# Optimization experiments

Measured on AMD Instinct MI355X. Metric: run time of the kernel, lower is better.

## Reference

```python
import jax, jax.numpy as jnp
import numpy as np

EPS = 1e-5

def _layernorm(h, g, b):
    m = jnp.mean(h, axis=-1, keepdims=True)
    v = jnp.mean((h - m) ** 2, axis=-1, keepdims=True)
    return (h - m) * jax.lax.rsqrt(v + EPS) * g + b

def setup_inputs() -> dict:
    key = jax.random.key(0)
    ks = jax.random.split(key, 12)
    B, C, T = 8, 512, 8192
    TOK, CD = 256, 768
    s = 0.02
    return {
        "x": jax.random.normal(ks[0], (B, C, T), dtype=jnp.float32),
        "context": jax.random.normal(ks[1], (B, TOK, CD), dtype=jnp.float32),
        "context_mask": jax.random.randint(ks[2], (B, TOK), 0, 2).astype(bool),
        "ln_g": jnp.ones((C,), jnp.float32),
        "ln_b": jnp.zeros((C,), jnp.float32),
        "cln_g": jnp.ones((CD,), jnp.float32),
        "cln_b": jnp.zeros((CD,), jnp.float32),
        "Wq": jax.random.normal(ks[3], (C, C), jnp.float32) * s,
        "bq": jnp.zeros((C,), jnp.float32),
        "Wk": jax.random.normal(ks[4], (C, CD), jnp.float32) * s,
        "bk": jnp.zeros((C,), jnp.float32),
        "Wv": jax.random.normal(ks[5], (C, CD), jnp.float32) * s,
        "bv": jnp.zeros((C,), jnp.float32),
    }

def reference(x, context, context_mask, ln_g, ln_b, cln_g, cln_b, Wq, bq, Wk, bk, Wv, bv):
    H = 8
    B, C, T = x.shape
    TOK = context.shape[1]
    D = C // H
    hidden = jnp.swapaxes(x, 1, 2)                     # [B, T, C]
    q = (_layernorm(hidden, ln_g, ln_b) @ Wq.T + bq).reshape(B, T, H, D)
    ctx_n = _layernorm(context, cln_g, cln_b)          # [B, TOK, CD]
    k = (ctx_n @ Wk.T + bk).reshape(B, TOK, H, D)
    v = (ctx_n @ Wv.T + bv).reshape(B, TOK, H, D)
    q = jax.nn.softmax(q, axis=-1)                     # feature map on queries
    m = context_mask[:, :, None, None]
    k = jnp.where(m, k, -jnp.finfo(k.dtype).max)
    v = v * m.astype(v.dtype)
    k = jax.nn.softmax(k, axis=1)                      # softmax over tokens
    attn = jnp.einsum('bnhd,bnhe->bhde', k, v)         # small [B,H,D,D] context matrix
    out = jnp.einsum('bthd,bhde->bthe', q, attn).reshape(B, T, C)
    return x + jnp.swapaxes(out, 1, 2)
```

## Files before the change

### kernel.cpp

```cpp
#include <hip/hip_runtime.h>

#define B_ 8
#define C_ 512
#define T_ 8192
#define TOK_ 256
#define CD_ 768

typedef __attribute__((ext_vector_type(8))) short bf16x8;
typedef __attribute__((ext_vector_type(4))) float f32x4;

__device__ __forceinline__ unsigned short f2bf(float f){
  union { float f; unsigned u; } v; v.f = f;
  return (unsigned short)((v.u + 0x7FFFu + ((v.u >> 16) & 1u)) >> 16);
}
__device__ __forceinline__ float bf2f(unsigned short h){
  union { unsigned u; float f; } v; v.u = ((unsigned)h) << 16;
  return v.f;
}

__global__ __launch_bounds__(256) void prep(const float* __restrict__ ctx,
    const float* __restrict__ cg_, const float* __restrict__ cb_,
    const float* __restrict__ Wq, const float* __restrict__ Wk, const float* __restrict__ Wv,
    unsigned short* __restrict__ ctx_nb, unsigned short* __restrict__ wq_pk,
    unsigned short* __restrict__ wkv_pk){
  __shared__ float rs[4][2];
  const int bid = blockIdx.x;
  const int tid = threadIdx.x;
  if (bid < 2048){
    const float* p = ctx + (size_t)bid * CD_;
    float s1 = 0.f, s2 = 0.f;
    for (int i = tid; i < CD_; i += 256){ float v = p[i]; s1 += v; s2 += v * v; }
    #pragma unroll
    for (int o = 32; o > 0; o >>= 1){ s1 += __shfl_xor(s1, o); s2 += __shfl_xor(s2, o); }
    if ((tid & 63) == 0){ rs[tid >> 6][0] = s1; rs[tid >> 6][1] = s2; }
    __syncthreads();
    s1 = rs[0][0] + rs[1][0] + rs[2][0] + rs[3][0];
    s2 = rs[0][1] + rs[1][1] + rs[2][1] + rs[3][1];
    float m = s1 / (float)CD_;
    float var = s2 / (float)CD_ - m * m;
    float rstd = rsqrtf(var + 1e-5f);
    unsigned short* q = ctx_nb + (size_t)bid * CD_;
    for (int i = tid; i < CD_; i += 256) q[i] = f2bf((p[i] - m) * rstd * cg_[i] + cb_[i]);
  } else if (bid < 2176){
    int slot = (bid - 2048) * 256 + tid;
    int ln = slot & 63, nt = (slot >> 6) & 31, kk = slot >> 11;
    int n  = nt * 16 + (ln & 15);
    int k0 = kk * 32 + (ln >> 4) * 8;
    bf16x8 v;
    #pragma unroll
    for (int j = 0; j < 8; j++) v[j] = (short)f2bf(Wq[(size_t)n * C_ + k0 + j]);
    *(bf16x8*)&wq_pk[(size_t)slot * 8] = v;
  } else {
    int slot = (bid - 2176) * 256 + tid;
    int ln = slot & 63, nt = (slot >> 6) & 7;
    int kkh = slot >> 9;
    int kk = kkh % 24, h = kkh / 24;
    const float* W = (nt < 4) ? Wk : Wv;
    int row = h * 64 + (nt & 3) * 16 + (ln & 15);
    int k0 = kk * 32 + (ln >> 4) * 8;
    bf16x8 v;
    #pragma unroll
    for (int j = 0; j < 8; j++) v[j] = (short)f2bf(W[(size_t)row * CD_ + k0 + j]);
    *(bf16x8*)&wkv_pk[(size_t)slot * 8] = v;
  }
}

__global__ __launch_bounds__(256) void ctx_attn(const unsigned short* __restrict__ ctx_nb,
    const unsigned short* __restrict__ wkv_pk,
    const float* __restrict__ bk, const float* __restrict__ bv,
    const int* __restrict__ mask, unsigned short* __restrict__ apk){
  __shared__ __align__(16) char smem[75776];
  unsigned short* a_st  = (unsigned short*)smem;
  unsigned short* p_lds = (unsigned short*)smem;
  unsigned short* v_lds = (unsigned short*)(smem + 32768);
  unsigned short* al    = (unsigned short*)(smem + 65536);
  float* wred = (float*)(smem + 73728);
  int* msk_l  = (int*)(smem + 74752);

  const int tid = threadIdx.x;
  const int b = blockIdx.x >> 3, h = blockIdx.x & 7;
  msk_l[tid] = mask[b * 256 + tid];

  const unsigned short* cb = ctx_nb + (size_t)b * 256 * CD_;
  const int w = tid >> 6, ln = tid & 63, lc = ln & 15, lk = ln >> 4;

  {
    const bf16x8* src = (const bf16x8*)(cb + (size_t)tid * CD_);
    #pragma unroll
    for (int s = 0; s < 4; s++){
      bf16x8 vv = src[s];
      *(bf16x8*)&a_st[(tid * 32 + s * 8) ^ ((tid & 7) << 3)] = vv;
    }
  }
  const bf16x8* wv_ = (const bf16x8*)wkv_pk;
  const size_t wbase = (size_t)h * 24 * 8 * 64;
  f32x4 acc[4][8];
  #pragma unroll
  for (int i = 0; i < 4; i++)
    #pragma unroll
    for (int j = 0; j < 8; j++) acc[i][j] = (f32x4){0.f,0.f,0.f,0.f};
  bf16x8 bbuf[2][8];
  #pragma unroll
  for (int nt = 0; nt < 8; nt++) bbuf[0][nt] = wv_[wbase + (size_t)(0 * 8 + nt) * 64 + ln];
  __syncthreads();

  for (int kk = 0; kk < 24; kk++){
    int cur = kk & 1;
    bf16x8 nx[4];
    if (kk < 23){
      const bf16x8* src = (const bf16x8*)(cb + (size_t)tid * CD_ + (kk + 1) * 32);
      #pragma unroll
      for (int s = 0; s < 4; s++) nx[s] = src[s];
      #pragma unroll
      for (int nt = 0; nt < 8; nt++)
        bbuf[cur ^ 1][nt] = wv_[wbase + (size_t)((kk + 1) * 8 + nt) * 64 + ln];
    }
    bf16x8 af[4];
    #pragma unroll
    for (int mt = 0; mt < 4; mt++){
      int row = w * 64 + mt * 16 + lc;
      af[mt] = *(const bf16x8*)&a_st[cur * 8192 + ((row * 32 + lk * 8) ^ ((row & 7) << 3))];
    }
    #pragma unroll
    for (int mt = 0; mt < 4; mt++)
      #pragma unroll
      for (int nt = 0; nt < 8; nt++)
        acc[mt][nt] = __builtin_amdgcn_mfma_f32_16x16x32_bf16(af[mt], bbuf[cur][nt], acc[mt][nt], 0, 0, 0);
    if (kk < 23){
      unsigned short* dst = a_st + (cur ^ 1) * 8192;
      #pragma unroll
      for (int s = 0; s < 4; s++)
        *(bf16x8*)&dst[(tid * 32 + s * 8) ^ ((tid & 7) << 3)] = nx[s];
    }
    __syncthreads();
  }

  float bia[8];
  #pragma unroll
  for (int nt = 0; nt < 8; nt++)
    bia[nt] = (nt < 4) ? bk[h * 64 + nt * 16 + lc] : bv[h * 64 + (nt - 4) * 16 + lc];
  bool mk[4][4];
  #pragma unroll
  for (int mt = 0; mt < 4; mt++)
    #pragma unroll
    for (int r = 0; r < 4; r++)
      mk[mt][r] = msk_l[w * 64 + mt * 16 + lk * 4 + r] != 0;

  float cred[4];
  #pragma unroll
  for (int nt = 0; nt < 4; nt++){
    float mx = -3.402823466e38f;
    #pragma unroll
    for (int mt = 0; mt < 4; mt++)
      #pragma unroll
      for (int r = 0; r < 4; r++)
        if (mk[mt][r]) mx = fmaxf(mx, acc[mt][nt][r] + bia[nt]);
    mx = fmaxf(mx, __shfl_xor(mx, 16));
    mx = fmaxf(mx, __shfl_xor(mx, 32));
    cred[nt] = mx;
  }
  if (lk == 0){
    #pragma unroll
    for (int nt = 0; nt < 4; nt++) wred[w * 64 + nt * 16 + lc] = cred[nt];
  }
  __syncthreads();
  float gmx[4];
  #pragma unroll
  for (int nt = 0; nt < 4; nt++){
    int d = nt * 16 + lc;
    gmx[nt] = fmaxf(fmaxf(wred[d], wred[64 + d]), fmaxf(wred[128 + d], wred[192 + d]));
  }
  __syncthreads();
  #pragma unroll
  for (int nt = 0; nt < 4; nt++){
    float s = 0.f;
    #pragma unroll
    for (int mt = 0; mt < 4; mt++)
      #pragma unroll
      for (int r = 0; r < 4; r++){
        float p = mk[mt][r] ? expf(acc[mt][nt][r] + bia[nt] - gmx[nt]) : 0.f;
        acc[mt][nt][r] = p;
        s += p;
      }
    s += __shfl_xor(s, 16);
    s += __shfl_xor(s, 32);
    cred[nt] = s;
  }
  if (lk == 0){
    #pragma unroll
    for (int nt = 0; nt < 4; nt++) wred[w * 64 + nt * 16 + lc] = cred[nt];
  }
  __syncthreads();
  float ginv[4];
  #pragma unroll
  for (int nt = 0; nt < 4; nt++){
    int d = nt * 16 + lc;
    float s = wred[d] + wred[64 + d] + wred[128 + d] + wred[192 + d];
    ginv[nt] = 1.0f / fmaxf(s, 1e-30f);
  }
  #pragma unroll
  for (int nt = 0; nt < 4; nt++){
    int d = nt * 16 + lc;
    #pragma unroll
    for (int mt = 0; mt < 4; mt++)
      #pragma unroll
      for (int r = 0; r < 4; r++){
        int n = w * 64 + mt * 16 + lk * 4 + r;
        p_lds[(d * 256 + n) ^ ((d & 7) << 3)] = f2bf(acc[mt][nt][r] * ginv[nt]);
      }
  }
  #pragma unroll
  for (int nt = 4; nt < 8; nt++){
    int e = (nt - 4) * 16 + lc;
    #pragma unroll
    for (int mt = 0; mt < 4; mt++)
      #pragma unroll
      for (int r = 0; r < 4; r++){
        int n = w * 64 + mt * 16 + lk * 4 + r;
        float vv = mk[mt][r] ? (acc[mt][nt][r] + bia[nt]) : 0.f;
        v_lds[(e * 256 + n) ^ ((e & 7) << 3)] = f2bf(vv);
      }
  }
  __syncthreads();

  f32x4 acc2[4];
  #pragma unroll
  for (int i = 0; i < 4; i++) acc2[i] = (f32x4){0.f,0.f,0.f,0.f};
  #pragma unroll
  for (int kk = 0; kk < 8; kk++){
    int d = w * 16 + lc;
    bf16x8 pa = *(const bf16x8*)&p_lds[(d * 256 + kk * 32 + lk * 8) ^ ((d & 7) << 3)];
    #pragma unroll
    for (int nt2 = 0; nt2 < 4; nt2++){
      int e = nt2 * 16 + lc;
      bf16x8 vb = *(const bf16x8*)&v_lds[(e * 256 + kk * 32 + lk * 8) ^ ((e & 7) << 3)];
      acc2[nt2] = __builtin_amdgcn_mfma_f32_16x16x32_bf16(pa, vb, acc2[nt2], 0, 0, 0);
    }
  }
  #pragma unroll
  for (int nt2 = 0; nt2 < 4; nt2++)
    #pragma unroll
    for (int r = 0; r < 4; r++)
      al[(w * 16 + lk * 4 + r) * 64 + nt2 * 16 + lc] = f2bf(acc2[nt2][r]);
  __syncthreads();

  #pragma unroll
  for (int s2 = 0; s2 < 2; s2++){
    int slot = s2 * 256 + tid;
    int l2 = slot & 63, nt = (slot >> 6) & 3, kk = slot >> 8;
    int e = nt * 16 + (l2 & 15), d0 = kk * 32 + (l2 >> 4) * 8;
    bf16x8 v;
    #pragma unroll
    for (int j = 0; j < 8; j++) v[j] = (short)al[(d0 + j) * 64 + e];
    *(bf16x8*)&apk[((size_t)(b * 8 + h) * 512 + slot) * 8] = v;
  }
}

__global__ __launch_bounds__(256, 3) void fused_main(const float* __restrict__ x,
    const float* __restrict__ g, const float* __restrict__ bl,
    const unsigned short* __restrict__ wq_pk, const float* __restrict__ bq,
    const unsigned short* __restrict__ attn_pk, float* __restrict__ out){
  __shared__ unsigned short a_lds[32 * 512];
  __shared__ float red[32 * 8 * 2];
  __shared__ float m_l[32], rs_l[32];
  const int tid = threadIdx.x;
  const int b = blockIdx.y;
  const int t0 = blockIdx.x * 32;
  const float* xb = x + (size_t)b * C_ * T_ + t0;
  const int t = tid & 31, cg = tid >> 5;

  unsigned int xr[32];
  {
    float s1 = 0.f, s2 = 0.f;
    #pragma unroll
    for (int jj = 0; jj < 32; jj++){
      float v0 = xb[(size_t)(cg * 64 + 2 * jj + 0) * T_ + t];
      float v1 = xb[(size_t)(cg * 64 + 2 * jj + 1) * T_ + t];
      s1 += v0 + v1; s2 += v0 * v0 + v1 * v1;
      xr[jj] = (unsigned)f2bf(v0) | ((unsigned)f2bf(v1) << 16);
    }
    red[(t * 8 + cg) * 2 + 0] = s1;
    red[(t * 8 + cg) * 2 + 1] = s2;
  }
  __syncthreads();
  if (tid < 32){
    float s1 = 0.f, s2 = 0.f;
    #pragma unroll
    for (int j = 0; j < 8; j++){ s1 += red[(tid*8+j)*2]; s2 += red[(tid*8+j)*2+1]; }
    float m = s1 * (1.0f / 512.0f);
    float var = s2 * (1.0f / 512.0f) - m * m;
    m_l[tid] = m;
    rs_l[tid] = rsqrtf(var + 1e-5f);
  }
  __syncthreads();
  {
    float m = m_l[t], rs = rs_l[t];
    #pragma unroll
    for (int o = 0; o < 8; o++){
      int c0 = cg * 64 + o * 8;
      bf16x8 av;
      #pragma unroll
      for (int j = 0; j < 8; j++){
        unsigned u = xr[o * 4 + (j >> 1)];
        float v = bf2f((unsigned short)((j & 1) ? (u >> 16) : (u & 0xffffu)));
        int c = c0 + j;
        av[j] = (short)f2bf((v - m) * rs * g[c] + bl[c]);
      }
      *(bf16x8*)&a_lds[(t * 512 + c0) ^ ((t & 7) << 3)] = av;
    }
  }
  __syncthreads();

  const int w = tid >> 6, ln = tid & 63, lc = ln & 15, lk = ln >> 4;
  f32x4 acc[2][8];
  #pragma unroll
  for (int i = 0; i < 2; i++)
    #pragma unroll
    for (int j = 0; j < 8; j++) acc[i][j] = (f32x4){0.f, 0.f, 0.f, 0.f};
  const bf16x8* wqv = (const bf16x8*)wq_pk;
  bf16x8 bbuf[2][8];
  #pragma unroll
  for (int nt = 0; nt < 8; nt++) bbuf[0][nt] = wqv[(size_t)(w * 8 + nt) * 64 + ln];
  #pragma unroll
  for (int kk = 0; kk < 16; kk++){
    int cur = kk & 1, nxt = cur ^ 1;
    if (kk < 15){
      #pragma unroll
      for (int nt = 0; nt < 8; nt++)
        bbuf[nxt][nt] = wqv[(size_t)((kk + 1) * 32 + w * 8 + nt) * 64 + ln];
    }
    bf16x8 af[2];
    #pragma unroll
    for (int mt = 0; mt < 2; mt++){
      int tr = mt * 16 + lc;
      af[mt] = *(const bf16x8*)&a_lds[(tr * 512 + kk * 32 + lk * 8) ^ ((tr & 7) << 3)];
    }
    #pragma unroll
    for (int mt = 0; mt < 2; mt++)
      #pragma unroll
      for (int nt = 0; nt < 8; nt++)
        acc[mt][nt] = __builtin_amdgcn_mfma_f32_16x16x32_bf16(af[mt], bbuf[cur][nt], acc[mt][nt], 0, 0, 0);
  }
  bf16x8 b2[2][2][4];
  const bf16x8* apk = (const bf16x8*)attn_pk;
  #pragma unroll
  for (int hh = 0; hh < 2; hh++)
    #pragma unroll
    for (int k2 = 0; k2 < 2; k2++)
      #pragma unroll
      for (int np = 0; np < 4; np++)
        b2[hh][k2][np] = apk[((size_t)(b * 8 + (2 * w + hh)) * 512 + (k2 * 4 + np) * 64 + ln)];
  float bqv[8];
  #pragma unroll
  for (int nt = 0; nt < 8; nt++) bqv[nt] = bq[w * 128 + nt * 16 + lc];
  #pragma unroll
  for (int mt = 0; mt < 2; mt++)
    #pragma unroll
    for (int r = 0; r < 4; r++)
      #pragma unroll
      for (int h2 = 0; h2 < 2; h2++){
        float v[4];
        #pragma unroll
        for (int j = 0; j < 4; j++) v[j] = acc[mt][h2 * 4 + j][r] + bqv[h2 * 4 + j];
        float mx = fmaxf(fmaxf(v[0], v[1]), fmaxf(v[2], v[3]));
        #pragma unroll
        for (int o = 1; o < 16; o <<= 1) mx = fmaxf(mx, __shfl_xor(mx, o));
        float e[4], s = 0.f;
        #pragma unroll
        for (int j = 0; j < 4; j++){ e[j] = expf(v[j] - mx); s += e[j]; }
        #pragma unroll
        for (int o = 1; o < 16; o <<= 1) s += __shfl_xor(s, o);
        float inv = 1.0f / s;
        #pragma unroll
        for (int j = 0; j < 4; j++) acc[mt][h2 * 4 + j][r] = e[j] * inv;
      }
  __syncthreads();
  #pragma unroll
  for (int mt = 0; mt < 2; mt++)
    #pragma unroll
    for (int r = 0; r < 4; r++){
      int tr = mt * 16 + lk * 4 + r;
      #pragma unroll
      for (int nt = 0; nt < 8; nt++){
        int col = w * 128 + nt * 16 + lc;
        a_lds[(tr * 512 + col) ^ ((tr & 7) << 3)] = f2bf(acc[mt][nt][r]);
      }
    }
  __syncthreads();
  f32x4 acc2[2][4][2];
  #pragma unroll
  for (int i = 0; i < 2; i++)
    #pragma unroll
    for (int j = 0; j < 4; j++)
      #pragma unroll
      for (int k = 0; k < 2; k++) acc2[i][j][k] = (f32x4){0.f, 0.f, 0.f, 0.f};
  #pragma unroll
  for (int k2 = 0; k2 < 2; k2++){
    bf16x8 pb[2][2];
    #pragma unroll
    for (int hh = 0; hh < 2; hh++)
      #pragma unroll
      for (int ntt = 0; ntt < 2; ntt++){
        int tr = ntt * 16 + lc;
        int col = w * 128 + hh * 64 + k2 * 32 + lk * 8;
        pb[hh][ntt] = *(const bf16x8*)&a_lds[(tr * 512 + col) ^ ((tr & 7) << 3)];
      }
    #pragma unroll
    for (int hh = 0; hh < 2; hh++)
      #pragma unroll
      for (int mtc = 0; mtc < 4; mtc++)
        #pragma unroll
        for (int ntt = 0; ntt < 2; ntt++)
          acc2[hh][mtc][ntt] = __builtin_amdgcn_mfma_f32_16x16x32_bf16(b2[hh][k2][mtc], pb[hh][ntt], acc2[hh][mtc][ntt], 0, 0, 0);
  }
  #pragma unroll
  for (int hh = 0; hh < 2; hh++)
    #pragma unroll
    for (int mtc = 0; mtc < 4; mtc++)
      #pragma unroll
      for (int ntt = 0; ntt < 2; ntt++)
        #pragma unroll
        for (int r = 0; r < 4; r++){
          int c = w * 128 + hh * 64 + mtc * 16 + lk * 4 + r;
          int tt2 = ntt * 16 + lc;
          float xv = xb[(size_t)c * T_ + tt2];
          out[((size_t)b * C_ + c) * T_ + t0 + tt2] = xv + acc2[hh][mtc][ntt][r];
        }
}

extern "C" void kernel_launch(void* const* d_in, const int* in_sizes, int n_in,
                              void* d_out, int out_size, void* d_ws, size_t ws_size,
                              hipStream_t stream) {
  (void)in_sizes; (void)n_in; (void)out_size; (void)ws_size;
  const float* x     = (const float*)d_in[0];
  const float* ctx   = (const float*)d_in[1];
  const int*   mask  = (const int*)d_in[2];
  const float* ln_g  = (const float*)d_in[3];
  const float* ln_b  = (const float*)d_in[4];
  const float* cln_g = (const float*)d_in[5];
  const float* cln_b = (const float*)d_in[6];
  const float* Wq    = (const float*)d_in[7];
  const float* bq    = (const float*)d_in[8];
  const float* Wk    = (const float*)d_in[9];
  const float* bk    = (const float*)d_in[10];
  const float* Wv    = (const float*)d_in[11];
  const float* bv    = (const float*)d_in[12];
  float* out = (float*)d_out;
  char* wsb = (char*)d_ws;
  unsigned short* ctx_nb = (unsigned short*)wsb;
  unsigned short* wq_pk  = (unsigned short*)(wsb + 3145728);
  unsigned short* wkv_pk = (unsigned short*)(wsb + 3670016);
  unsigned short* apk    = (unsigned short*)(wsb + 5242880);

  prep<<<2560, 256, 0, stream>>>(ctx, cln_g, cln_b, Wq, Wk, Wv, ctx_nb, wq_pk, wkv_pk);
  ctx_attn<<<64, 256, 0, stream>>>(ctx_nb, wkv_pk, bk, bv, mask, apk);
  fused_main<<<dim3(T_ / 32, B_), 256, 0, stream>>>(x, ln_g, ln_b, wq_pk, bq, apk, out);
}
```

Measured before the change: 356.5 us.

## Double token tile to 64 per block with 512 threads and float2 loads

The main fused kernel now processes 64 tokens per block with 8 waves arranged as 2 token-rows by 4 column groups, instead of 32 tokens with 4 waves. The x load for layernorm statistics uses float2 loads of two adjacent tokens, and the reduction buffer is padded to 17 to avoid LDS bank conflicts. The aim is to halve the number of blocks, get better coalescing on the strided x reads, and amortize the Wq and attention-matrix fragment loads over more tokens. In exchange, LDS per block doubles to about 64KB and launch bounds rise to 512 threads with 4 blocks per CU requested, which could limit occupancy or increase register pressure.

```diff
diff --git a/kernel.cpp b/kernel.cpp
--- a/kernel.cpp
+++ b/kernel.cpp
@@ -256,37 +256,44 @@
   }
 }
 
-__global__ __launch_bounds__(256, 3) void fused_main(const float* __restrict__ x,
+__global__ __launch_bounds__(512, 4) void fused_main(const float* __restrict__ x,
     const float* __restrict__ g, const float* __restrict__ bl,
     const unsigned short* __restrict__ wq_pk, const float* __restrict__ bq,
     const unsigned short* __restrict__ attn_pk, float* __restrict__ out){
-  __shared__ unsigned short a_lds[32 * 512];
-  __shared__ float red[32 * 8 * 2];
-  __shared__ float m_l[32], rs_l[32];
+  __shared__ unsigned short a_lds[64 * 512];
+  __shared__ float red2[64 * 17 * 2];
+  __shared__ float m_l[64], rs_l[64];
   const int tid = threadIdx.x;
   const int b = blockIdx.y;
-  const int t0 = blockIdx.x * 32;
+  const int t0 = blockIdx.x * 64;
   const float* xb = x + (size_t)b * C_ * T_ + t0;
-  const int t = tid & 31, cg = tid >> 5;
+  const int tp = tid & 31, cg = tid >> 5;
+  const int t2 = tp * 2;
 
   unsigned int xr[32];
   {
+    float s1a = 0.f, s2a = 0.f, s1b = 0.f, s2b = 0.f;
+    #pragma unroll
+    for (int j = 0; j < 32; j++){
+      int c = cg * 32 + j;
+      float2 v = *(const float2*)&xb[(size_t)c * T_ + t2];
+      s1a += v.x; s2a += v.x * v.x;
+      s1b += v.y; s2b += v.y * v.y;
+      xr[j] = (unsigned)f2bf(v.x) | ((unsigned)f2bf(v.y) << 16);
+    }
+    red2[(t2 * 17 + cg) * 2 + 0] = s1a;
+    red2[(t2 * 17 + cg) * 2 + 1] = s2a;
+    red2[((t2 + 1) * 17 + cg) * 2 + 0] = s1b;
+    red2[((t2 + 1) * 17 + cg) * 2 + 1] = s2b;
+  }
+  __syncthreads();
+  if (tid < 64){
     float s1 = 0.f, s2 = 0.f;
     #pragma unroll
-    for (int jj = 0; jj < 32; jj++){
-      float v0 = xb[(size_t)(cg * 64 + 2 * jj + 0) * T_ + t];
-      float v1 = xb[(size_t)(cg * 64 + 2 * jj + 1) * T_ + t];
-      s1 += v0 + v1; s2 += v0 * v0 + v1 * v1;
-      xr[jj] = (unsigned)f2bf(v0) | ((unsigned)f2bf(v1) << 16);
-    }
-    red[(t * 8 + cg) * 2 + 0] = s1;
-    red[(t * 8 + cg) * 2 + 1] = s2;
-  }
-  __syncthreads();
-  if (tid < 32){
-    float s1 = 0.f, s2 = 0.f;
-    #pragma unroll
-    for (int j = 0; j < 8; j++){ s1 += red[(tid*8+j)*2]; s2 += red[(tid*8+j)*2+1]; }
+    for (int j = 0; j < 16; j++){
+      s1 += red2[(tid * 17 + j) * 2 + 0];
+      s2 += red2[(tid * 17 + j) * 2 + 1];
+    }
     float m = s1 * (1.0f / 512.0f);
     float var = s2 * (1.0f / 512.0f) - m * m;
     m_l[tid] = m;
@@ -294,24 +301,28 @@
   }
   __syncthreads();
   {
-    float m = m_l[t], rs = rs_l[t];
-    #pragma unroll
-    for (int o = 0; o < 8; o++){
-      int c0 = cg * 64 + o * 8;
-      bf16x8 av;
+    float m0 = m_l[t2], rs0 = rs_l[t2];
+    float m1 = m_l[t2 + 1], rs1 = rs_l[t2 + 1];
+    #pragma unroll
+    for (int o = 0; o < 4; o++){
+      int c0 = cg * 32 + o * 8;
+      bf16x8 av0, av1;
       #pragma unroll
       for (int j = 0; j < 8; j++){
-        unsigned u = xr[o * 4 + (j >> 1)];
-        float v = bf2f((unsigned short)((j & 1) ? (u >> 16) : (u & 0xffffu)));
+        unsigned u = xr[o * 8 + j];
         int c = c0 + j;
-        av[j] = (short)f2bf((v - m) * rs * g[c] + bl[c]);
-      }
-      *(bf16x8*)&a_lds[(t * 512 + c0) ^ ((t & 7) << 3)] = av;
+        float gv = g[c], bv2 = bl[c];
+        av0[j] = (short)f2bf((bf2f((unsigned short)(u & 0xffffu)) - m0) * rs0 * gv + bv2);
+        av1[j] = (short)f2bf((bf2f((unsigned short)(u >> 16)) - m1) * rs1 * gv + bv2);
+      }
+      *(bf16x8*)&a_lds[(t2 * 512 + c0) ^ ((t2 & 7) << 3)] = av0;
+      *(bf16x8*)&a_lds[((t2 + 1) * 512 + c0) ^ (((t2 + 1) & 7) << 3)] = av1;
     }
   }
   __syncthreads();
 
   const int w = tid >> 6, ln = tid & 63, lc = ln & 15, lk = ln >> 4;
+  const int wr = w >> 2, wc = w & 3;
   f32x4 acc[2][8];
   #pragma unroll
   for (int i = 0; i < 2; i++)
@@ -320,19 +331,19 @@
   const bf16x8* wqv = (const bf16x8*)wq_pk;
   bf16x8 bbuf[2][8];
   #pragma unroll
-  for (int nt = 0; nt < 8; nt++) bbuf[0][nt] = wqv[(size_t)(w * 8 + nt) * 64 + ln];
+  for (int nt = 0; nt < 8; nt++) bbuf[0][nt] = wqv[(size_t)(wc * 8 + nt) * 64 + ln];
   #pragma unroll
   for (int kk = 0; kk < 16; kk++){
     int cur = kk & 1, nxt = cur ^ 1;
     if (kk < 15){
       #pragma unroll
       for (int nt = 0; nt < 8; nt++)
-        bbuf[nxt][nt] = wqv[(size_t)((kk + 1) * 32 + w * 8 + nt) * 64 + ln];
+        bbuf[nxt][nt] = wqv[(size_t)((kk + 1) * 32 + wc * 8 + nt) * 64 + ln];
     }
     bf16x8 af[2];
     #pragma unroll
     for (int mt = 0; mt < 2; mt++){
-      int tr = mt * 16 + lc;
+      int tr = wr * 32 + mt * 16 + lc;
       af[mt] = *(const bf16x8*)&a_lds[(tr * 512 + kk * 32 + lk * 8) ^ ((tr & 7) << 3)];
     }
     #pragma unroll
@@ -349,10 +360,10 @@
     for (int k2 = 0; k2 < 2; k2++)
       #pragma unroll
       for (int np = 0; np < 4; np++)
-        b2[hh][k2][np] = apk[((size_t)(b * 8 + (2 * w + hh)) * 512 + (k2 * 4 + np) * 64 + ln)];
+        b2[hh][k2][np] = apk[((size_t)(b * 8 + (2 * wc + hh)) * 512 + (k2 * 4 + np) * 64 + ln)];
   float bqv[8];
   #pragma unroll
-  for (int nt = 0; nt < 8; nt++) bqv[nt] = bq[w * 128 + nt * 16 + lc];
+  for (int nt = 0; nt < 8; nt++) bqv[nt] = bq[wc * 128 + nt * 16 + lc];
   #pragma unroll
   for (int mt = 0; mt < 2; mt++)
     #pragma unroll
@@ -379,10 +390,10 @@
   for (int mt = 0; mt < 2; mt++)
     #pragma unroll
     for (int r = 0; r < 4; r++){
-      int tr = mt * 16 + lk * 4 + r;
+      int tr = wr * 32 + mt * 16 + lk * 4 + r;
       #pragma unroll
       for (int nt = 0; nt < 8; nt++){
-        int col = w * 128 + nt * 16 + lc;
+        int col = wc * 128 + nt * 16 + lc;
         a_lds[(tr * 512 + col) ^ ((tr & 7) << 3)] = f2bf(acc[mt][nt][r]);
       }
     }
@@ -401,8 +412,8 @@
     for (int hh = 0; hh < 2; hh++)
       #pragma unroll
       for (int ntt = 0; ntt < 2; ntt++){
-        int tr = ntt * 16 + lc;
-        int col = w * 128 + hh * 64 + k2 * 32 + lk * 8;
+        int tr = wr * 32 + ntt * 16 + lc;
+        int col = wc * 128 + hh * 64 + k2 * 32 + lk * 8;
         pb[hh][ntt] = *(const bf16x8*)&a_lds[(tr * 512 + col) ^ ((tr & 7) << 3)];
       }
     #pragma unroll
@@ -421,8 +432,8 @@
       for (int ntt = 0; ntt < 2; ntt++)
         #pragma unroll
         for (int r = 0; r < 4; r++){
-          int c = w * 128 + hh * 64 + mtc * 16 + lk * 4 + r;
-          int tt2 = ntt * 16 + lc;
+          int c = wc * 128 + hh * 64 + mtc * 16 + lk * 4 + r;
+          int tt2 = wr * 32 + ntt * 16 + lc;
           float xv = xb[(size_t)c * T_ + tt2];
           out[((size_t)b * C_ + c) * T_ + t0 + tt2] = xv + acc2[hh][mtc][ntt][r];
         }
@@ -454,5 +465,5 @@
 
   prep<<<2560, 256, 0, stream>>>(ctx, cln_g, cln_b, Wq, Wk, Wv, ctx_nb, wq_pk, wkv_pk);
   ctx_attn<<<64, 256, 0, stream>>>(ctx_nb, wkv_pk, bk, bv, mask, apk);
-  fused_main<<<dim3(T_ / 32, B_), 256, 0, stream>>>(x, ln_g, ln_b, wq_pk, bq, apk, out);
-}
+  fused_main<<<dim3(T_ / 64, B_), 512, 0, stream>>>(x, ln_g, ln_b, wq_pk, bq, apk, out);
+}
```

Result: slower. 703.2 us (+97.3%).
